# Kernel tuning notes

Hardware: AMD Instinct MI355X
Metric: run time of the kernel (lower is better)

The kernel has to match this reference:

```python
import jax, jax.numpy as jnp
import numpy as np

N_STEPS = 64          # sample['N']
G = 1.0               # sample['g'] (constant diffusion)
NUM_SAMPLES = 2       # num_samples_per_obs
W_SCALE = 0.05

# interpolant coefficients: alpha(s)=1-s, beta(s)=s, sigma(s)=1-s
# derivatives: alpha_dot=-1, beta_dot=1, sigma_dot=-1

def b_net(x, x0, s, W1, b1, W2, b2, W3, b3):
    # B_net(interpolant, current_state, s): MLP on concat([x, x0, s])
    sf = jnp.full(x.shape[:-1] + (1,), s, dtype=x.dtype)
    inp = jnp.concatenate([x, x0, sf], axis=-1)      # [B, 2*dim+1]
    h = jax.nn.relu(inp @ W1 + b1)
    h = jax.nn.relu(h @ W2 + b2)
    return h @ W3 + b3                                # [B, dim]


def setup_inputs() -> dict:
    key = jax.random.key(0)
    ks = jax.random.split(key, 4)
    num_obs, dim, hid = 65536, 64, 256
    X0 = jax.random.normal(ks[0], (num_obs, dim), dtype=jnp.float32)
    W1 = jax.random.normal(ks[1], (2 * dim + 1, hid), dtype=jnp.float32) * W_SCALE
    W2 = jax.random.normal(ks[2], (hid, hid), dtype=jnp.float32) * W_SCALE
    W3 = jax.random.normal(ks[3], (hid, dim), dtype=jnp.float32) * W_SCALE
    return {
        "X0": X0,
        "W1": W1, "b1": jnp.zeros((hid,), jnp.float32),
        "W2": W2, "b2": jnp.zeros((hid,), jnp.float32),
        "W3": W3, "b3": jnp.zeros((dim,), jnp.float32),
    }


def reference(X0, W1, b1, W2, b2, W3, b3):
    time = jnp.linspace(0.0, 1.0, N_STEPS + 1, dtype=X0.dtype)
    ds = jnp.asarray(1.0 / N_STEPS, X0.dtype)
    sqrt_ds = jnp.sqrt(ds)
    params = (W1, b1, W2, b2, W3, b3)

    def sample_one(key):
        k0, kloop = jax.random.split(key)
        # first Euler step: X = X0 + ds*B(X0,X0,0) + sigma(0)*sqrt(ds)*eta
        eta0 = jax.random.normal(k0, X0.shape, X0.dtype)
        X = X0 + ds * b_net(X0, X0, time[0], *params) + (1.0 - time[0]) * sqrt_ds * eta0

        def step(carry, n):
            X, key = carry
            key, kn = jax.random.split(key)
            s = time[n]
            al, ald = 1.0 - s, -1.0
            bt, btd = s, 1.0
            sg, sgd = 1.0 - s, -1.0
            drift_b = b_net(X, X0, s, *params)
            # score correction (self.score)
            c = btd * X + (bt * ald - btd * al) * X0
            A = 1.0 / (s * sg * (btd * sg - bt * sgd))
            score = A * (bt * drift_b - c)
            # adjusted drift: drift + 0.5*(g^2 - sigma^2)*score
            control = 0.5 * (G ** 2 - sg ** 2) * score
            eta = jax.random.normal(kn, X.shape, X.dtype)
            X = X + ds * (drift_b + control) + G * sqrt_ds * eta
            return (X, key), None

        (X, _), _ = jax.lax.scan(step, (X, kloop), jnp.arange(1, N_STEPS))
        return X

    keys = jax.random.split(jax.random.key(1), NUM_SAMPLES)
    samples = jax.vmap(sample_one)(keys)   # [num_samples, num_obs, dim]
    return samples
```

## Files before the change

### kernel.cpp

```cpp
#include <hip/hip_runtime.h>
#include <stdint.h>


#define PARTITIONABLE 1

namespace {

constexpr int   kObs    = 65536;
constexpr int   kDim    = 64;
constexpr int   kSteps  = 64;
constexpr float kDs     = 1.0f / 64.0f;
constexpr float kSqrtDs = 0.125f;

constexpr int kWeightBytes = 256 * 1024;
constexpr int kKeysOff     = kWeightBytes;
constexpr int kStabOff     = kKeysOff + 1024;

typedef _Float16 f16x8 __attribute__((ext_vector_type(8)));
typedef _Float16 f16x4 __attribute__((ext_vector_type(4)));
typedef float    f32x4 __attribute__((ext_vector_type(4)));

#define MFMA16(a, b, c) __builtin_amdgcn_mfma_f32_16x16x32_f16((a), (b), (c), 0, 0, 0)

__device__ __forceinline__ uint32_t rotl(uint32_t v, int r) {
  return (v << r) | (v >> (32 - r));
}

__device__ __forceinline__ void tf2x32(uint32_t k0, uint32_t k1,
                                       uint32_t& x0, uint32_t& x1) {
  uint32_t k2 = k0 ^ k1 ^ 0x1BD11BDAu;
  x0 += k0; x1 += k1;
  x0 += x1; x1 = rotl(x1, 13); x1 ^= x0;
  x0 += x1; x1 = rotl(x1, 15); x1 ^= x0;
  x0 += x1; x1 = rotl(x1, 26); x1 ^= x0;
  x0 += x1; x1 = rotl(x1,  6); x1 ^= x0;
  x0 += k1; x1 += k2 + 1u;
  x0 += x1; x1 = rotl(x1, 17); x1 ^= x0;
  x0 += x1; x1 = rotl(x1, 29); x1 ^= x0;
  x0 += x1; x1 = rotl(x1, 16); x1 ^= x0;
  x0 += x1; x1 = rotl(x1, 24); x1 ^= x0;
  x0 += k2; x1 += k0 + 2u;
  x0 += x1; x1 = rotl(x1, 13); x1 ^= x0;
  x0 += x1; x1 = rotl(x1, 15); x1 ^= x0;
  x0 += x1; x1 = rotl(x1, 26); x1 ^= x0;
  x0 += x1; x1 = rotl(x1,  6); x1 ^= x0;
  x0 += k0; x1 += k1 + 3u;
  x0 += x1; x1 = rotl(x1, 17); x1 ^= x0;
  x0 += x1; x1 = rotl(x1, 29); x1 ^= x0;
  x0 += x1; x1 = rotl(x1, 16); x1 ^= x0;
  x0 += x1; x1 = rotl(x1, 24); x1 ^= x0;
  x0 += k1; x1 += k2 + 4u;
  x0 += x1; x1 = rotl(x1, 13); x1 ^= x0;
  x0 += x1; x1 = rotl(x1, 15); x1 ^= x0;
  x0 += x1; x1 = rotl(x1, 26); x1 ^= x0;
  x0 += x1; x1 = rotl(x1,  6); x1 ^= x0;
  x0 += k2; x1 += k0 + 5u;
}

__device__ __forceinline__ void jax_split(uint32_t k0, uint32_t k1,
                                          uint32_t& a0, uint32_t& a1,
                                          uint32_t& b0, uint32_t& b1) {
#if PARTITIONABLE
  uint32_t x0 = 0u, x1 = 0u; tf2x32(k0, k1, x0, x1); a0 = x0; a1 = x1;
  uint32_t y0 = 0u, y1 = 1u; tf2x32(k0, k1, y0, y1); b0 = y0; b1 = y1;
#else
  uint32_t x0 = 0u, x1 = 2u; tf2x32(k0, k1, x0, x1);
  uint32_t y0 = 1u, y1 = 3u; tf2x32(k0, k1, y0, y1);
  a0 = x0; a1 = y0; b0 = x1; b1 = y1;
#endif
}

__device__ __forceinline__ uint32_t draw_bits(uint32_t k0, uint32_t k1, uint32_t i) {
#if PARTITIONABLE
  uint32_t x0 = 0u, x1 = i;
  tf2x32(k0, k1, x0, x1);
  return x0 ^ x1;
#else
  const uint32_t half = (uint32_t)kObs * kDim / 2;
  if (i < half) {
    uint32_t x0 = i, x1 = i + half; tf2x32(k0, k1, x0, x1); return x0;
  } else {
    uint32_t x0 = i - half, x1 = i; tf2x32(k0, k1, x0, x1); return x1;
  }
#endif
}

__device__ __forceinline__ float erfinv32s(float x) {
  float w = -__logf(fmaf(-x, x, 1.0f));
  float p;
  if (w < 5.0f) {
    w = w - 2.5f;
    p =            3.974239e-08f;
    p = fmaf(p, w, 4.854653e-07f);
    p = fmaf(p, w, -4.982823e-06f);
    p = fmaf(p, w, -6.210533e-06f);
    p = fmaf(p, w, 3.091202e-04f);
    p = fmaf(p, w, -1.773035e-03f);
    p = fmaf(p, w, -5.908134e-03f);
    p = fmaf(p, w, 3.488027e-01f);
    p = fmaf(p, w, 2.1233135f);
  } else {
    w = sqrtf(w) - 3.0f;
    p =            -2.8314694e-04f;
    p = fmaf(p, w, 1.4276561e-04f);
    p = fmaf(p, w, 1.908261e-03f);
    p = fmaf(p, w, -5.1950111e-03f);
    p = fmaf(p, w, 8.1168903e-03f);
    p = fmaf(p, w, -1.07797888e-02f);
    p = fmaf(p, w, 1.33485780e-02f);
    p = fmaf(p, w, 1.4165811f);
    p = fmaf(p, w, 4.0064343f);
  }
  return p * x;
}

__device__ __forceinline__ float bits_to_normal(uint32_t bits) {
  const float lo = -0.99999994f;
  float f = __uint_as_float(0x3f800000u | (bits >> 9)) - 1.0f;
  float u = fmaxf(lo, fmaf(f, 2.0f, lo));
  return erfinv32s(u);
}

}

__global__ void prep_weights(const float* __restrict__ W1,
                             const float* __restrict__ W2,
                             const float* __restrict__ W3,
                             _Float16* __restrict__ ws) {
  const int G = blockIdx.x;
  const int t = threadIdx.x;

  if (G >= 256) {
    if (t < 2) {
      uint32_t* kout = (uint32_t*)((char*)ws + kKeysOff) + t * 128;
      uint32_t s0a, s0b, s1a, s1b;
      jax_split(0u, 1u, s0a, s0b, s1a, s1b);
      const uint32_t sk0 = t ? s1a : s0a;
      const uint32_t sk1 = t ? s1b : s0b;
      uint32_t kd0, kd1, kl0, kl1;
      jax_split(sk0, sk1, kd0, kd1, kl0, kl1);
      kout[0] = kd0; kout[1] = kd1;
      for (int n = 1; n < kSteps; ++n) {
        uint32_t na, nb, xa, xb;
        jax_split(kl0, kl1, na, nb, xa, xb);
        kl0 = na; kl1 = nb;
        kout[2 * n] = xa; kout[2 * n + 1] = xb;
      }
    }
    if (t < kSteps) {
      const float s  = (float)t * kDs;
      const float sg = 1.0f - s;
      f32x4 v;
      v[0] = s;
      v[1] = (t == 0) ? 0.0f : 1.0f / (s * sg);
      v[2] = 0.5f * (1.0f - sg * sg);
      v[3] = kDs * v[2] * v[1];
      *(f32x4*)((char*)ws + kStabOff + t * 16) = v;
    }
    return;
  }

  const int lane = t >> 2;
  const int j0   = (t & 3) * 2;
  const int w    = G >> 5;
  const int T    = G & 31;
  const int lm   = lane & 15;
  const int kb   = (lane >> 4) << 3;

#pragma unroll
  for (int jj = 0; jj < 2; ++jj) {
    const int j = j0 + jj;
    float v;
    if (T < 8) {
      const int mt = T >> 2, kt = T & 3;
      const int col = w * 32 + mt * 16 + lm;
      const int k   = kt * 32 + kb + j;
      v = W1[k * 256 + col];
    } else if (T < 24) {
      const int u = T - 8;
      const int mt = u >> 3, kt = u & 7;
      const int col = w * 32 + mt * 16 + lm;
      const int k   = kt * 32 + kb + j;
      v = W2[k * 256 + col];
    } else {
      const int kt  = T - 24;
      const int col = (w >> 1) * 16 + lm;
      const int k   = kt * 32 + kb + j;
      v = W3[k * 64 + col];
    }
    ws[(size_t)G * 512 + lane * 8 + j] = (_Float16)v;
  }
}

__global__ __launch_bounds__(512, 2)
void sde_mfma(const float* __restrict__ X0g,
              const float* __restrict__ W1,
              const float* __restrict__ b1,
              const float* __restrict__ b2,
              const float* __restrict__ b3,
              const _Float16* __restrict__ ws,
              float* __restrict__ out) {
  __shared__ alignas(16) char  xAf [8 * 1024];
  __shared__ alignas(16) char  h1f [32 * 1024];
  __shared__ alignas(16) char  h2f [32 * 1024];
  __shared__ alignas(16) float bb  [832];

  const int t    = threadIdx.x;
  const int w    = t >> 6;
  const int l    = t & 63;
  const int lq   = l >> 4;
  const int lm   = l & 15;
  const int samp = blockIdx.x >> 10;
  const int tile = blockIdx.x & 1023;
  const int r0   = tile * 64;
  const int mt3  = w >> 1;
  const int rpar = w & 1;
  const int d0   = mt3 * 16 + lq * 4;

  const int rb  = l * 16;
  const int lo1 = ((lq >> 1) * 16 + lm) * 16 + (lq & 1) * 8;
  const int kt3 = mt3 >> 1;
  const int ln3 = (((mt3 & 1) * 2 + (lq >> 1)) * 16 + lm) * 16 + (lq & 1) * 8;

  if (t < 256) {
    bb[t]       = b1[t];
    bb[256 + t] = W1[128 * 256 + t];
    bb[512 + t] = b2[t];
  } else if (t < 320) {
    bb[768 + (t - 256)] = b3[t - 256];
  }

  {
    const int li = t >> 3;
    const int ci = (t & 7) * 8;
    const float* p = X0g + (size_t)(r0 + li) * kDim + ci;
    const float4 a = *(const float4*)p;
    const float4 b = *(const float4*)(p + 4);
    f16x8 h;
    h[0] = (_Float16)a.x; h[1] = (_Float16)a.y;
    h[2] = (_Float16)a.z; h[3] = (_Float16)a.w;
    h[4] = (_Float16)b.x; h[5] = (_Float16)b.y;
    h[6] = (_Float16)b.z; h[7] = (_Float16)b.w;
    const int fa = ((ci >> 5) * 4 + (li >> 4)) * 1024 +
                   (((ci >> 3) & 3) * 16 + (li & 15)) * 16;
    *(f16x8*)(xAf + fa) = h;
    *(f16x8*)(h1f + fa) = h;
  }

  float xv[2][4];
  f32x4 x0q[2];
#pragma unroll
  for (int h = 0; h < 2; ++h) {
    const int row = (2 * h + rpar) * 16 + lm;
    x0q[h] = *(const f32x4*)(X0g + (size_t)(r0 + row) * kDim + d0);
#pragma unroll
    for (int q = 0; q < 4; ++q) xv[h][q] = x0q[h][q];
  }
  const uint32_t giH0 = (uint32_t)((r0 + rpar * 16 + lm) * kDim + d0);
  const uint32_t giH1 = giH0 + 32u * kDim;

  const char* pW = (const char*)ws + (size_t)w * 32768 + l * 16;
  f16x8 wL1[2][2], wx0[2][2], wL2[16], wL3[8];
#pragma unroll
  for (int mt = 0; mt < 2; ++mt) {
    wL1[mt][0] = *(const f16x8*)(pW + (mt * 4 + 0) * 1024);
    wL1[mt][1] = *(const f16x8*)(pW + (mt * 4 + 1) * 1024);
    wx0[mt][0] = *(const f16x8*)(pW + (mt * 4 + 2) * 1024);
    wx0[mt][1] = *(const f16x8*)(pW + (mt * 4 + 3) * 1024);
  }
#pragma unroll
  for (int i = 0; i < 16; ++i) wL2[i] = *(const f16x8*)(pW + (8 + i) * 1024);
#pragma unroll
  for (int i = 0; i < 8; ++i)  wL3[i] = *(const f16x8*)(pW + (24 + i) * 1024);

  const uint32_t* keys = (const uint32_t*)((const char*)ws + kKeysOff) + samp * 128;
  const f32x4*    stab = (const f32x4*)((const char*)ws + kStabOff);

  __syncthreads();

  f16x4 pre[4][2];
#pragma unroll
  for (int nt = 0; nt < 4; ++nt) {
    const f16x8 xf0 = *(const f16x8*)(h1f + (0 * 4 + nt) * 1024 + rb);
    const f16x8 xf1 = *(const f16x8*)(h1f + (1 * 4 + nt) * 1024 + rb);
#pragma unroll
    for (int mt = 0; mt < 2; ++mt) {
      f32x4 p = {0.f, 0.f, 0.f, 0.f};
      p = MFMA16(wx0[mt][0], xf0, p);
      p = MFMA16(wx0[mt][1], xf1, p);
      f16x4 ph;
#pragma unroll
      for (int q = 0; q < 4; ++q) ph[q] = (_Float16)p[q];
      pre[nt][mt] = ph;
    }
  }
  __syncthreads();

  auto L1C = [&](int h, float sv) {
#pragma unroll
    for (int j = 0; j < 2; ++j) {
      const int nt = 2 * h + j;
      const f16x8 bf0 = *(const f16x8*)(xAf + (0 * 4 + nt) * 1024 + rb);
      const f16x8 bf1 = *(const f16x8*)(xAf + (1 * 4 + nt) * 1024 + rb);
#pragma unroll
      for (int mt = 0; mt < 2; ++mt) {
        f32x4 c = {0.f, 0.f, 0.f, 0.f};
        c = MFMA16(wL1[mt][0], bf0, c);
        c = MFMA16(wL1[mt][1], bf1, c);
        const int nb = w * 32 + mt * 16 + lq * 4;
        const f32x4 bq = *(const f32x4*)&bb[nb];
        const f32x4 wq = *(const f32x4*)&bb[256 + nb];
        const f16x4 ph = pre[nt][mt];
        f16x4 o;
#pragma unroll
        for (int q = 0; q < 4; ++q)
          o[q] = (_Float16)fmaxf(c[q] + (float)ph[q] + fmaf(sv, wq[q], bq[q]), 0.f);
        *(f16x4*)(h1f + (w * 4 + nt) * 1024 + mt * 512 + lo1) = o;
      }
    }
  };

  auto L2C = [&](int h) {
    f32x4 c[2][2];
#pragma unroll
    for (int mt = 0; mt < 2; ++mt)
#pragma unroll
      for (int ni = 0; ni < 2; ++ni)
        c[mt][ni] = (f32x4){0.f, 0.f, 0.f, 0.f};
#pragma unroll
    for (int kh = 0; kh < 2; ++kh) {
      f16x8 bh[2][4];
#pragma unroll
      for (int ni = 0; ni < 2; ++ni)
#pragma unroll
        for (int k4 = 0; k4 < 4; ++k4)
          bh[ni][k4] = *(const f16x8*)
              (h1f + ((kh * 4 + k4) * 4 + 2 * h + ni) * 1024 + rb);
#pragma unroll
      for (int mt = 0; mt < 2; ++mt)
#pragma unroll
        for (int k4 = 0; k4 < 4; ++k4) {
          const f16x8 aW = wL2[mt * 8 + kh * 4 + k4];
          c[mt][0] = MFMA16(aW, bh[0][k4], c[mt][0]);
          c[mt][1] = MFMA16(aW, bh[1][k4], c[mt][1]);
        }
    }
#pragma unroll
    for (int mt = 0; mt < 2; ++mt) {
      const int nb = w * 32 + mt * 16 + lq * 4;
      const f32x4 bq = *(const f32x4*)&bb[512 + nb];
#pragma unroll
      for (int ni = 0; ni < 2; ++ni) {
        f16x4 o;
#pragma unroll
        for (int q = 0; q < 4; ++q)
          o[q] = (_Float16)fmaxf(c[mt][ni][q] + bq[q], 0.f);
        *(f16x4*)(h2f + (w * 4 + 2 * h + ni) * 1024 + mt * 512 + lo1) = o;
      }
    }
  };

  auto L3U = [&](int h, const float* eta, float sv, float Pv) {
    const int rt = 2 * h + rpar;
    f32x4 dA = {0.f, 0.f, 0.f, 0.f}, dB = {0.f, 0.f, 0.f, 0.f};
#pragma unroll
    for (int kh = 0; kh < 2; ++kh) {
      f16x8 bh[4];
#pragma unroll
      for (int k4 = 0; k4 < 4; ++k4)
        bh[k4] = *(const f16x8*)(h2f + ((kh * 4 + k4) * 4 + rt) * 1024 + rb);
      dA = MFMA16(wL3[kh * 4 + 0], bh[0], dA);
      dB = MFMA16(wL3[kh * 4 + 1], bh[1], dB);
      dA = MFMA16(wL3[kh * 4 + 2], bh[2], dA);
      dB = MFMA16(wL3[kh * 4 + 3], bh[3], dB);
    }
    const f32x4 b3q = *(const f32x4*)&bb[768 + d0];
    f16x4 hx;
#pragma unroll
    for (int q = 0; q < 4; ++q) {
      const float ov = dA[q] + dB[q] + b3q[q];
      const float t1 = fmaf(sv, ov, x0q[h][q] - xv[h][q]);
      float nx = fmaf(kSqrtDs, eta[q], xv[h][q]);
      nx = fmaf(kDs, ov, nx);
      nx = fmaf(Pv, t1, nx);
      xv[h][q] = nx;
      hx[q] = (_Float16)nx;
    }
    *(f16x4*)(xAf + (kt3 * 4 + rt) * 1024 + ln3) = hx;
  };

  L1C(0, stab[0][0]);
  __syncthreads();

  float et0[4], et1[4];
  for (int n = 0; n < kSteps; ++n) {
    const f32x4 st = stab[n];
    const float s = st[0], P = st[3];
    const uint32_t ka = keys[2 * n], kb = keys[2 * n + 1];

    L2C(0);
    L1C(1, s);
#pragma unroll
    for (int q = 0; q < 4; ++q)
      et0[q] = bits_to_normal(draw_bits(ka, kb, giH0 + q));
    __syncthreads();

    L2C(1);
    L3U(0, et0, s, P);
#pragma unroll
    for (int q = 0; q < 4; ++q)
      et1[q] = bits_to_normal(draw_bits(ka, kb, giH1 + q));
    __syncthreads();

    if (n + 1 < kSteps) L1C(0, stab[n + 1][0]);
    L3U(1, et1, s, P);
    __syncthreads();
  }

#pragma unroll
  for (int h = 0; h < 2; ++h) {
    const int row = (2 * h + rpar) * 16 + lm;
    const size_t ob = (size_t)samp * ((size_t)kObs * kDim) +
                      (size_t)(r0 + row) * kDim + d0;
    f32x4 v;
#pragma unroll
    for (int q = 0; q < 4; ++q) v[q] = xv[h][q];
    *(f32x4*)(out + ob) = v;
  }
}

extern "C" void kernel_launch(void* const* d_in, const int* in_sizes, int n_in,
                              void* d_out, int out_size, void* d_ws, size_t ws_size,
                              hipStream_t stream) {
  const float* X0 = (const float*)d_in[0];
  const float* W1 = (const float*)d_in[1];
  const float* b1 = (const float*)d_in[2];
  const float* W2 = (const float*)d_in[3];
  const float* b2 = (const float*)d_in[4];
  const float* W3 = (const float*)d_in[5];
  const float* b3 = (const float*)d_in[6];
  _Float16* ws = (_Float16*)d_ws;

  prep_weights<<<dim3(257), dim3(256), 0, stream>>>(W1, W2, W3, ws);
  sde_mfma<<<dim3(2048), dim3(512), 0, stream>>>(X0, W1, b1, b2, b3, ws,
                                                 (float*)d_out);
}
```

Baseline: 2.830 ms.

## Halve block to 4 waves on 32 rows, keep W3 in LDS

The SDE kernel now runs 256-thread blocks, each handling 32 rows instead of 64, with 4096 blocks. Each wave owns a 64-column slice of layers 1 and 2, so more weights per wave live in registers (32 W2 fragments). The W3 weights move from registers to a shared-memory copy loaded once per block. The prep kernel repacks weights to match this layout. The per-step schedule becomes three serial phases (L1, L2, L3 update) with barriers in between, replacing the previous interleaved half-tile pipeline. This trades away the overlap between layers for smaller blocks, and it raises register pressure per wave in exchange for less duplicated weight traffic.

Measured after the change: 3.514 ms. 1.24x slower.

```diff
diff --git a/kernel.cpp b/kernel.cpp
--- a/kernel.cpp
+++ b/kernel.cpp
@@ -12,9 +12,9 @@
 constexpr float kDs     = 1.0f / 64.0f;
 constexpr float kSqrtDs = 0.125f;
 
-constexpr int kWeightBytes = 256 * 1024;
-constexpr int kKeysOff     = kWeightBytes;
-constexpr int kStabOff     = kKeysOff + 1024;
+constexpr int kW3Off   = 192 * 1024;
+constexpr int kKeysOff = 224 * 1024;
+constexpr int kStabOff = kKeysOff + 1024;
 
 typedef _Float16 f16x8 __attribute__((ext_vector_type(8)));
 typedef _Float16 f16x4 __attribute__((ext_vector_type(4)));
@@ -130,7 +130,7 @@
   const int G = blockIdx.x;
   const int t = threadIdx.x;
 
-  if (G >= 256) {
+  if (G >= 224) {
     if (t < 2) {
       uint32_t* kout = (uint32_t*)((char*)ws + kKeysOff) + t * 128;
       uint32_t s0a, s0b, s1a, s1b;
@@ -162,8 +162,6 @@
 
   const int lane = t >> 2;
   const int j0   = (t & 3) * 2;
-  const int w    = G >> 5;
-  const int T    = G & 31;
   const int lm   = lane & 15;
   const int kb   = (lane >> 4) << 3;
 
@@ -171,20 +169,31 @@
   for (int jj = 0; jj < 2; ++jj) {
     const int j = j0 + jj;
     float v;
-    if (T < 8) {
-      const int mt = T >> 2, kt = T & 3;
-      const int col = w * 32 + mt * 16 + lm;
-      const int k   = kt * 32 + kb + j;
-      v = W1[k * 256 + col];
-    } else if (T < 24) {
-      const int u = T - 8;
+    if (G < 192) {
+      const int w = G / 48;
+      const int T = G % 48;
+      if (T < 8) {
+        const int mt = T >> 1, kt = T & 1;
+        const int col = w * 64 + mt * 16 + lm;
+        const int k   = kt * 32 + kb + j;
+        v = W1[k * 256 + col];
+      } else if (T < 16) {
+        const int u = T - 8;
+        const int mt = u >> 1, kt = u & 1;
+        const int col = w * 64 + mt * 16 + lm;
+        const int k   = 64 + kt * 32 + kb + j;
+        v = W1[k * 256 + col];
+      } else {
+        const int u = T - 16;
+        const int mt = u >> 3, kt = u & 7;
+        const int col = w * 64 + mt * 16 + lm;
+        const int k   = kt * 32 + kb + j;
+        v = W2[k * 256 + col];
+      }
+    } else {
+      const int u  = G - 192;
       const int mt = u >> 3, kt = u & 7;
-      const int col = w * 32 + mt * 16 + lm;
-      const int k   = kt * 32 + kb + j;
-      v = W2[k * 256 + col];
-    } else {
-      const int kt  = T - 24;
-      const int col = (w >> 1) * 16 + lm;
+      const int col = mt * 16 + lm;
       const int k   = kt * 32 + kb + j;
       v = W3[k * 64 + col];
     }
@@ -192,7 +201,7 @@
   }
 }
 
-__global__ __launch_bounds__(512, 2)
+__global__ __launch_bounds__(256, 2)
 void sde_mfma(const float* __restrict__ X0g,
               const float* __restrict__ W1,
               const float* __restrict__ b1,
@@ -200,9 +209,10 @@
               const float* __restrict__ b3,
               const _Float16* __restrict__ ws,
               float* __restrict__ out) {
-  __shared__ alignas(16) char  xAf [8 * 1024];
-  __shared__ alignas(16) char  h1f [32 * 1024];
-  __shared__ alignas(16) char  h2f [32 * 1024];
+  __shared__ alignas(16) char  xAf [4 * 1024];
+  __shared__ alignas(16) char  h1f [16 * 1024];
+  __shared__ alignas(16) char  h2f [16 * 1024];
+  __shared__ alignas(16) char  w3f [32 * 1024];
   __shared__ alignas(16) float bb  [832];
 
   const int t    = threadIdx.x;
@@ -210,25 +220,19 @@
   const int l    = t & 63;
   const int lq   = l >> 4;
   const int lm   = l & 15;
-  const int samp = blockIdx.x >> 10;
-  const int tile = blockIdx.x & 1023;
-  const int r0   = tile * 64;
-  const int mt3  = w >> 1;
-  const int rpar = w & 1;
-  const int d0   = mt3 * 16 + lq * 4;
+  const int samp = blockIdx.x >> 11;
+  const int tile = blockIdx.x & 2047;
+  const int r0   = tile * 32;
+  const int d0   = w * 16 + lq * 4;
 
   const int rb  = l * 16;
   const int lo1 = ((lq >> 1) * 16 + lm) * 16 + (lq & 1) * 8;
-  const int kt3 = mt3 >> 1;
-  const int ln3 = (((mt3 & 1) * 2 + (lq >> 1)) * 16 + lm) * 16 + (lq & 1) * 8;
-
-  if (t < 256) {
-    bb[t]       = b1[t];
-    bb[256 + t] = W1[128 * 256 + t];
-    bb[512 + t] = b2[t];
-  } else if (t < 320) {
-    bb[768 + (t - 256)] = b3[t - 256];
-  }
+  const int ln3 = (((w & 1) * 2 + (lq >> 1)) * 16 + lm) * 16 + (lq & 1) * 8;
+
+  bb[t]       = b1[t];
+  bb[256 + t] = W1[128 * 256 + t];
+  bb[512 + t] = b2[t];
+  if (t < 64) bb[768 + t] = b3[t];
 
   {
     const int li = t >> 3;
@@ -241,190 +245,186 @@
     h[2] = (_Float16)a.z; h[3] = (_Float16)a.w;
     h[4] = (_Float16)b.x; h[5] = (_Float16)b.y;
     h[6] = (_Float16)b.z; h[7] = (_Float16)b.w;
-    const int fa = ((ci >> 5) * 4 + (li >> 4)) * 1024 +
+    const int fa = ((ci >> 5) * 2 + (li >> 4)) * 1024 +
                    (((ci >> 3) & 3) * 16 + (li & 15)) * 16;
     *(f16x8*)(xAf + fa) = h;
     *(f16x8*)(h1f + fa) = h;
   }
 
+#pragma unroll
+  for (int j = 0; j < 8; ++j)
+    *(f16x8*)(w3f + j * 4096 + t * 16) =
+        *(const f16x8*)((const char*)ws + kW3Off + j * 4096 + t * 16);
+
   float xv[2][4];
   f32x4 x0q[2];
 #pragma unroll
-  for (int h = 0; h < 2; ++h) {
-    const int row = (2 * h + rpar) * 16 + lm;
-    x0q[h] = *(const f32x4*)(X0g + (size_t)(r0 + row) * kDim + d0);
-#pragma unroll
-    for (int q = 0; q < 4; ++q) xv[h][q] = x0q[h][q];
-  }
-  const uint32_t giH0 = (uint32_t)((r0 + rpar * 16 + lm) * kDim + d0);
-  const uint32_t giH1 = giH0 + 32u * kDim;
-
-  const char* pW = (const char*)ws + (size_t)w * 32768 + l * 16;
-  f16x8 wL1[2][2], wx0[2][2], wL2[16], wL3[8];
-#pragma unroll
-  for (int mt = 0; mt < 2; ++mt) {
-    wL1[mt][0] = *(const f16x8*)(pW + (mt * 4 + 0) * 1024);
-    wL1[mt][1] = *(const f16x8*)(pW + (mt * 4 + 1) * 1024);
-    wx0[mt][0] = *(const f16x8*)(pW + (mt * 4 + 2) * 1024);
-    wx0[mt][1] = *(const f16x8*)(pW + (mt * 4 + 3) * 1024);
-  }
-#pragma unroll
-  for (int i = 0; i < 16; ++i) wL2[i] = *(const f16x8*)(pW + (8 + i) * 1024);
-#pragma unroll
-  for (int i = 0; i < 8; ++i)  wL3[i] = *(const f16x8*)(pW + (24 + i) * 1024);
+  for (int rt = 0; rt < 2; ++rt) {
+    const int row = rt * 16 + lm;
+    x0q[rt] = *(const f32x4*)(X0g + (size_t)(r0 + row) * kDim + d0);
+#pragma unroll
+    for (int q = 0; q < 4; ++q) xv[rt][q] = x0q[rt][q];
+  }
+  const uint32_t giA = (uint32_t)((r0 + lm) * kDim + d0);
+  const uint32_t giB = giA + 16u * kDim;
+
+  const char* pW = (const char*)ws + (size_t)w * 48 * 1024 + l * 16;
+  f16x8 wL1[4][2], wL2[32];
+#pragma unroll
+  for (int mt = 0; mt < 4; ++mt) {
+    wL1[mt][0] = *(const f16x8*)(pW + (mt * 2 + 0) * 1024);
+    wL1[mt][1] = *(const f16x8*)(pW + (mt * 2 + 1) * 1024);
+  }
+#pragma unroll
+  for (int i = 0; i < 32; ++i)
+    wL2[i] = *(const f16x8*)(pW + (16 + i) * 1024);
 
   const uint32_t* keys = (const uint32_t*)((const char*)ws + kKeysOff) + samp * 128;
   const f32x4*    stab = (const f32x4*)((const char*)ws + kStabOff);
 
   __syncthreads();
 
-  f16x4 pre[4][2];
-#pragma unroll
-  for (int nt = 0; nt < 4; ++nt) {
-    const f16x8 xf0 = *(const f16x8*)(h1f + (0 * 4 + nt) * 1024 + rb);
-    const f16x8 xf1 = *(const f16x8*)(h1f + (1 * 4 + nt) * 1024 + rb);
-#pragma unroll
-    for (int mt = 0; mt < 2; ++mt) {
-      f32x4 p = {0.f, 0.f, 0.f, 0.f};
-      p = MFMA16(wx0[mt][0], xf0, p);
-      p = MFMA16(wx0[mt][1], xf1, p);
-      f16x4 ph;
-#pragma unroll
-      for (int q = 0; q < 4; ++q) ph[q] = (_Float16)p[q];
-      pre[nt][mt] = ph;
+  f16x4 pre[2][4];
+  {
+    f16x8 wx0[4][2];
+#pragma unroll
+    for (int mt = 0; mt < 4; ++mt) {
+      wx0[mt][0] = *(const f16x8*)(pW + (8 + mt * 2 + 0) * 1024);
+      wx0[mt][1] = *(const f16x8*)(pW + (8 + mt * 2 + 1) * 1024);
+    }
+#pragma unroll
+    for (int rt = 0; rt < 2; ++rt) {
+      const f16x8 xf0 = *(const f16x8*)(h1f + (0 * 2 + rt) * 1024 + rb);
+      const f16x8 xf1 = *(const f16x8*)(h1f + (1 * 2 + rt) * 1024 + rb);
+#pragma unroll
+      for (int mt = 0; mt < 4; ++mt) {
+        f32x4 p = {0.f, 0.f, 0.f, 0.f};
+        p = MFMA16(wx0[mt][0], xf0, p);
+        p = MFMA16(wx0[mt][1], xf1, p);
+        f16x4 ph;
+#pragma unroll
+        for (int q = 0; q < 4; ++q) ph[q] = (_Float16)p[q];
+        pre[rt][mt] = ph;
+      }
     }
   }
   __syncthreads();
 
-  auto L1C = [&](int h, float sv) {
-#pragma unroll
-    for (int j = 0; j < 2; ++j) {
-      const int nt = 2 * h + j;
-      const f16x8 bf0 = *(const f16x8*)(xAf + (0 * 4 + nt) * 1024 + rb);
-      const f16x8 bf1 = *(const f16x8*)(xAf + (1 * 4 + nt) * 1024 + rb);
-#pragma unroll
-      for (int mt = 0; mt < 2; ++mt) {
+  for (int n = 0; n < kSteps; ++n) {
+    const f32x4 st = stab[n];
+    const float s = st[0], P = st[3];
+    const uint32_t ka = keys[2 * n], kbk = keys[2 * n + 1];
+
+    float et0[4];
+#pragma unroll
+    for (int q = 0; q < 4; ++q)
+      et0[q] = bits_to_normal(draw_bits(ka, kbk, giA + q));
+
+#pragma unroll
+    for (int rt = 0; rt < 2; ++rt) {
+      const f16x8 bf0 = *(const f16x8*)(xAf + (0 * 2 + rt) * 1024 + rb);
+      const f16x8 bf1 = *(const f16x8*)(xAf + (1 * 2 + rt) * 1024 + rb);
+#pragma unroll
+      for (int mt = 0; mt < 4; ++mt) {
         f32x4 c = {0.f, 0.f, 0.f, 0.f};
         c = MFMA16(wL1[mt][0], bf0, c);
         c = MFMA16(wL1[mt][1], bf1, c);
-        const int nb = w * 32 + mt * 16 + lq * 4;
+        const int nb = w * 64 + mt * 16 + lq * 4;
         const f32x4 bq = *(const f32x4*)&bb[nb];
         const f32x4 wq = *(const f32x4*)&bb[256 + nb];
-        const f16x4 ph = pre[nt][mt];
+        const f16x4 ph = pre[rt][mt];
         f16x4 o;
 #pragma unroll
         for (int q = 0; q < 4; ++q)
-          o[q] = (_Float16)fmaxf(c[q] + (float)ph[q] + fmaf(sv, wq[q], bq[q]), 0.f);
-        *(f16x4*)(h1f + (w * 4 + nt) * 1024 + mt * 512 + lo1) = o;
-      }
-    }
-  };
-
-  auto L2C = [&](int h) {
-    f32x4 c[2][2];
-#pragma unroll
-    for (int mt = 0; mt < 2; ++mt)
-#pragma unroll
-      for (int ni = 0; ni < 2; ++ni)
-        c[mt][ni] = (f32x4){0.f, 0.f, 0.f, 0.f};
-#pragma unroll
-    for (int kh = 0; kh < 2; ++kh) {
-      f16x8 bh[2][4];
-#pragma unroll
-      for (int ni = 0; ni < 2; ++ni)
+          o[q] = (_Float16)fmaxf(c[q] + (float)ph[q] + fmaf(s, wq[q], bq[q]), 0.f);
+        *(f16x4*)(h1f + ((w * 2 + (mt >> 1)) * 2 + rt) * 1024 +
+                  (mt & 1) * 512 + lo1) = o;
+      }
+    }
+    __syncthreads();
+
+    float et1[4];
+#pragma unroll
+    for (int rt = 0; rt < 2; ++rt) {
+      f32x4 c[4];
+#pragma unroll
+      for (int mt = 0; mt < 4; ++mt) c[mt] = (f32x4){0.f, 0.f, 0.f, 0.f};
+#pragma unroll
+      for (int kh = 0; kh < 2; ++kh) {
+        f16x8 bh[4];
 #pragma unroll
         for (int k4 = 0; k4 < 4; ++k4)
-          bh[ni][k4] = *(const f16x8*)
-              (h1f + ((kh * 4 + k4) * 4 + 2 * h + ni) * 1024 + rb);
-#pragma unroll
-      for (int mt = 0; mt < 2; ++mt)
+          bh[k4] = *(const f16x8*)
+              (h1f + ((kh * 4 + k4) * 2 + rt) * 1024 + rb);
+#pragma unroll
+        for (int k4 = 0; k4 < 4; ++k4)
+#pragma unroll
+          for (int mt = 0; mt < 4; ++mt)
+            c[mt] = MFMA16(wL2[mt * 8 + kh * 4 + k4], bh[k4], c[mt]);
+      }
+      if (rt == 0) {
+#pragma unroll
+        for (int q = 0; q < 4; ++q)
+          et1[q] = bits_to_normal(draw_bits(ka, kbk, giB + q));
+      }
+#pragma unroll
+      for (int mt = 0; mt < 4; ++mt) {
+        const int nb = w * 64 + mt * 16 + lq * 4;
+        const f32x4 bq = *(const f32x4*)&bb[512 + nb];
+        f16x4 o;
+#pragma unroll
+        for (int q = 0; q < 4; ++q)
+          o[q] = (_Float16)fmaxf(c[mt][q] + bq[q], 0.f);
+        *(f16x4*)(h2f + ((w * 2 + (mt >> 1)) * 2 + rt) * 1024 +
+                  (mt & 1) * 512 + lo1) = o;
+      }
+    }
+    __syncthreads();
+
+    const f32x4 b3q = *(const f32x4*)&bb[768 + d0];
+#pragma unroll
+    for (int rt = 0; rt < 2; ++rt) {
+      f32x4 dA = {0.f, 0.f, 0.f, 0.f}, dB = {0.f, 0.f, 0.f, 0.f};
+#pragma unroll
+      for (int kh = 0; kh < 2; ++kh) {
+        f16x8 bh[4], wf[4];
 #pragma unroll
         for (int k4 = 0; k4 < 4; ++k4) {
-          const f16x8 aW = wL2[mt * 8 + kh * 4 + k4];
-          c[mt][0] = MFMA16(aW, bh[0][k4], c[mt][0]);
-          c[mt][1] = MFMA16(aW, bh[1][k4], c[mt][1]);
+          bh[k4] = *(const f16x8*)
+              (h2f + ((kh * 4 + k4) * 2 + rt) * 1024 + rb);
+          wf[k4] = *(const f16x8*)
+              (w3f + (w * 8 + kh * 4 + k4) * 1024 + rb);
         }
-    }
-#pragma unroll
-    for (int mt = 0; mt < 2; ++mt) {
-      const int nb = w * 32 + mt * 16 + lq * 4;
-      const f32x4 bq = *(const f32x4*)&bb[512 + nb];
-#pragma unroll
-      for (int ni = 0; ni < 2; ++ni) {
-        f16x4 o;
-#pragma unroll
-        for (int q = 0; q < 4; ++q)
-          o[q] = (_Float16)fmaxf(c[mt][ni][q] + bq[q], 0.f);
-        *(f16x4*)(h2f + (w * 4 + 2 * h + ni) * 1024 + mt * 512 + lo1) = o;
-      }
-    }
-  };
-
-  auto L3U = [&](int h, const float* eta, float sv, float Pv) {
-    const int rt = 2 * h + rpar;
-    f32x4 dA = {0.f, 0.f, 0.f, 0.f}, dB = {0.f, 0.f, 0.f, 0.f};
-#pragma unroll
-    for (int kh = 0; kh < 2; ++kh) {
-      f16x8 bh[4];
-#pragma unroll
-      for (int k4 = 0; k4 < 4; ++k4)
-        bh[k4] = *(const f16x8*)(h2f + ((kh * 4 + k4) * 4 + rt) * 1024 + rb);
-      dA = MFMA16(wL3[kh * 4 + 0], bh[0], dA);
-      dB = MFMA16(wL3[kh * 4 + 1], bh[1], dB);
-      dA = MFMA16(wL3[kh * 4 + 2], bh[2], dA);
-      dB = MFMA16(wL3[kh * 4 + 3], bh[3], dB);
-    }
-    const f32x4 b3q = *(const f32x4*)&bb[768 + d0];
-    f16x4 hx;
-#pragma unroll
-    for (int q = 0; q < 4; ++q) {
-      const float ov = dA[q] + dB[q] + b3q[q];
-      const float t1 = fmaf(sv, ov, x0q[h][q] - xv[h][q]);
-      float nx = fmaf(kSqrtDs, eta[q], xv[h][q]);
-      nx = fmaf(kDs, ov, nx);
-      nx = fmaf(Pv, t1, nx);
-      xv[h][q] = nx;
-      hx[q] = (_Float16)nx;
-    }
-    *(f16x4*)(xAf + (kt3 * 4 + rt) * 1024 + ln3) = hx;
-  };
-
-  L1C(0, stab[0][0]);
-  __syncthreads();
-
-  float et0[4], et1[4];
-  for (int n = 0; n < kSteps; ++n) {
-    const f32x4 st = stab[n];
-    const float s = st[0], P = st[3];
-    const uint32_t ka = keys[2 * n], kb = keys[2 * n + 1];
-
-    L2C(0);
-    L1C(1, s);
-#pragma unroll
-    for (int q = 0; q < 4; ++q)
-      et0[q] = bits_to_normal(draw_bits(ka, kb, giH0 + q));
+        dA = MFMA16(wf[0], bh[0], dA);
+        dB = MFMA16(wf[1], bh[1], dB);
+        dA = MFMA16(wf[2], bh[2], dA);
+        dB = MFMA16(wf[3], bh[3], dB);
+      }
+      f16x4 hx;
+#pragma unroll
+      for (int q = 0; q < 4; ++q) {
+        const float ov  = dA[q] + dB[q] + b3q[q];
+        const float eta = rt ? et1[q] : et0[q];
+        const float t1  = fmaf(s, ov, x0q[rt][q] - xv[rt][q]);
+        float nx = fmaf(kSqrtDs, eta, xv[rt][q]);
+        nx = fmaf(kDs, ov, nx);
+        nx = fmaf(P, t1, nx);
+        xv[rt][q] = nx;
+        hx[q] = (_Float16)nx;
+      }
+      *(f16x4*)(xAf + ((w >> 1) * 2 + rt) * 1024 + ln3) = hx;
+    }
     __syncthreads();
-
-    L2C(1);
-    L3U(0, et0, s, P);
-#pragma unroll
-    for (int q = 0; q < 4; ++q)
-      et1[q] = bits_to_normal(draw_bits(ka, kb, giH1 + q));
-    __syncthreads();
-
-    if (n + 1 < kSteps) L1C(0, stab[n + 1][0]);
-    L3U(1, et1, s, P);
-    __syncthreads();
-  }
-
-#pragma unroll
-  for (int h = 0; h < 2; ++h) {
-    const int row = (2 * h + rpar) * 16 + lm;
+  }
+
+#pragma unroll
+  for (int rt = 0; rt < 2; ++rt) {
+    const int row = rt * 16 + lm;
     const size_t ob = (size_t)samp * ((size_t)kObs * kDim) +
                       (size_t)(r0 + row) * kDim + d0;
     f32x4 v;
 #pragma unroll
-    for (int q = 0; q < 4; ++q) v[q] = xv[h][q];
+    for (int q = 0; q < 4; ++q) v[q] = xv[rt][q];
     *(f32x4*)(out + ob) = v;
   }
 }
@@ -441,7 +441,7 @@
   const float* b3 = (const float*)d_in[6];
   _Float16* ws = (_Float16*)d_ws;
 
-  prep_weights<<<dim3(257), dim3(256), 0, stream>>>(W1, W2, W3, ws);
-  sde_mfma<<<dim3(2048), dim3(512), 0, stream>>>(X0, W1, b1, b2, b3, ws,
+  prep_weights<<<dim3(225), dim3(256), 0, stream>>>(W1, W2, W3, ws);
+  sde_mfma<<<dim3(4096), dim3(256), 0, stream>>>(X0, W1, b1, b2, b3, ws,
                                                  (float*)d_out);
 }
```
